# Optimization experiments

Hardware: AMD Instinct MI355X
Metric: run time of the kernel (lower is better)

## Reference

```python
import jax, jax.numpy as jnp
import numpy as np

D_MODEL = 1024
HEAD = 16


def setup_inputs() -> dict:
    key = jax.random.key(0)
    ks = jax.random.split(key, 11)
    B, S, D = 2, 2048, D_MODEL
    s = 1.0 / np.sqrt(D)
    return {
        "query": jax.random.normal(ks[0], (B, S, D), jnp.float32),
        "value": jax.random.normal(ks[1], (B, S, D), jnp.float32),
        "key": jax.random.normal(ks[2], (B, S, D), jnp.float32),
        "Wq_w": jax.random.normal(ks[3], (D, D), jnp.float32) * s,
        "Wq_b": jnp.zeros((D,), jnp.float32),
        "Wk_w": jax.random.normal(ks[4], (D, D), jnp.float32) * s,
        "Wk_b": jnp.zeros((D,), jnp.float32),
        "Wv_w": jax.random.normal(ks[5], (D, D), jnp.float32) * s,
        "Wv_b": jnp.zeros((D,), jnp.float32),
        "Wo_w": jax.random.normal(ks[6], (D, D), jnp.float32) * s,
        "Wo_b": jnp.zeros((D,), jnp.float32),
    }


def reference(query, value, key, Wq_w, Wq_b, Wk_w, Wk_b, Wv_w, Wv_b, Wo_w, Wo_b):
    B, S, D = query.shape
    H = HEAD
    kd = D // H
    # Linear projections (torch Linear: x @ W.T + b)
    Q = query @ Wq_w.T + Wq_b
    K = key @ Wk_w.T + Wk_b
    V = value @ Wv_w.T + Wv_b
    # [B, S, D] -> [B, H, S, kd]
    Q = Q.reshape(B, S, H, kd).transpose(0, 2, 1, 3)
    K = K.reshape(B, S, H, kd).transpose(0, 2, 1, 3)
    V = V.reshape(B, S, H, kd).transpose(0, 2, 1, 3)
    scale = 1.0 / jnp.sqrt(jnp.asarray(kd, query.dtype))
    score = jnp.einsum("bhqd,bhkd->bhqk", Q, K) * scale  # [B,H,S,S]
    attn = jax.nn.softmax(score, axis=-1)
    x = jnp.einsum("bhqk,bhkd->bhqd", attn, V)  # [B,H,S,kd]
    x = x.transpose(0, 2, 1, 3).reshape(B, S, D)
    return x @ Wo_w.T + Wo_b
```

## Files before the change

### kernel.cpp

```cpp
#include <hip/hip_runtime.h>
#include <stdint.h>
#include <stddef.h>


typedef __attribute__((ext_vector_type(8))) short short8;
typedef __attribute__((ext_vector_type(4))) float floatx4;
typedef __attribute__((ext_vector_type(16))) float f32x16;
typedef __attribute__((ext_vector_type(4))) unsigned short ushort4v;

#define MFMA16(a, b, c) __builtin_amdgcn_mfma_f32_16x16x32_bf16((a), (b), (c), 0, 0, 0)
#define MFMA32(a, b, c) __builtin_amdgcn_mfma_f32_32x32x16_bf16((a), (b), (c), 0, 0, 0)

#define CL2 0.18033688011112042f

__device__ __forceinline__ unsigned short f2bf(float f) {
  union { float f; unsigned u; } v; v.f = f;
  unsigned u = v.u;
  return (unsigned short)((u + 0x7fffu + ((u >> 16) & 1u)) >> 16);
}

__device__ __forceinline__ float fast_exp2(float x) {
  float r;
  asm("v_exp_f32 %0, %1" : "=v"(r) : "v"(x));
  return r;
}

__device__ __forceinline__ unsigned cvt_pk_bf16(float lo, float hi) {
  unsigned r;
  asm("v_cvt_pk_bf16_f32 %0, %1, %2" : "=v"(r) : "v"(lo), "v"(hi));
  return r;
}

#define PSWAP(a, b) asm("v_permlane32_swap_b32 %0, %1" : "+v"(a), "+v"(b))

#define WAITBAR(N) do { \
  asm volatile("s_waitcnt vmcnt(" #N ")" ::: "memory"); \
  __builtin_amdgcn_s_barrier(); \
  __builtin_amdgcn_sched_barrier(0); \
} while (0)

union B8 { unsigned short s[8]; short8 v; };
union U4 { unsigned w[4]; short8 v; };

__device__ __forceinline__ void gload_lds16(const unsigned short* g, unsigned short* l) {
  __builtin_amdgcn_global_load_lds(
      (__attribute__((address_space(1))) void*)(g),
      (__attribute__((address_space(3))) void*)(l), 16, 0, 0);
}

__global__ __launch_bounds__(256) void convert_all(
    const float* __restrict__ q, const float* __restrict__ k, const float* __restrict__ v,
    const float* __restrict__ wq, const float* __restrict__ wk,
    const float* __restrict__ wv, const float* __restrict__ wo,
    unsigned short* __restrict__ qb, unsigned short* __restrict__ kb,
    unsigned short* __restrict__ vb, unsigned short* __restrict__ w4)
{
  int b = blockIdx.x;
  const float* s; unsigned short* d;
  float sc = 1.0f;
  if (b < 2048)      { s = q;  d = qb; }
  else if (b < 4096) { s = k;  d = kb; b -= 2048; }
  else if (b < 6144) { s = v;  d = vb; b -= 4096; }
  else if (b < 6656) { s = wq; d = w4;            b -= 6144; sc = CL2; }
  else if (b < 7168) { s = wk; d = w4 + 1048576;  b -= 6656; }
  else if (b < 7680) { s = wv; d = w4 + 2097152;  b -= 7168; }
  else               { s = wo; d = w4 + 3145728;  b -= 7680; }
  const size_t i = ((size_t)b * 256 + threadIdx.x) * 8;
  float4 f0 = *(const float4*)(s + i);
  float4 f1 = *(const float4*)(s + i + 4);
  B8 u;
  u.s[0] = f2bf(f0.x * sc); u.s[1] = f2bf(f0.y * sc);
  u.s[2] = f2bf(f0.z * sc); u.s[3] = f2bf(f0.w * sc);
  u.s[4] = f2bf(f1.x * sc); u.s[5] = f2bf(f1.y * sc);
  u.s[6] = f2bf(f1.z * sc); u.s[7] = f2bf(f1.w * sc);
  *(short8*)(d + i) = u.v;
}

__global__ __launch_bounds__(256) void proj_gemm(
    const unsigned short* __restrict__ A0, const unsigned short* __restrict__ A1,
    const unsigned short* __restrict__ A2, const unsigned short* __restrict__ W4,
    const float* __restrict__ b0, const float* __restrict__ b1, const float* __restrict__ b2,
    unsigned short* __restrict__ Qp, unsigned short* __restrict__ Kp,
    unsigned short* __restrict__ Vt)
{
  const int z = blockIdx.z;
  const unsigned short* A = (z == 0) ? A0 : ((z == 1) ? A1 : A2);
  const unsigned short* W = W4 + (size_t)z * 1048576;
  const float* bias = (z == 0) ? b0 : ((z == 1) ? b1 : b2);
  const float esc = (z == 0) ? CL2 : 1.0f;

  const int m0 = blockIdx.y * 128;
  const int n0 = blockIdx.x * 128;
  const int tid = threadIdx.x;
  const int lane = tid & 63;
  const int wid = tid >> 6;
  const int wr = wid >> 1, wc = wid & 1;
  const int g = lane >> 4, l15 = lane & 15;

  __shared__ unsigned short As[3][128 * 32];
  __shared__ unsigned short Bs[3][128 * 32];

  const floatx4 vzero = {0.f, 0.f, 0.f, 0.f};
  floatx4 acc[4][4];
#pragma unroll
  for (int i = 0; i < 4; ++i)
#pragma unroll
    for (int j = 0; j < 4; ++j) acc[i][j] = vzero;

  const int lr = lane >> 2;
  const int lc = (lane & 3) * 8;
  const unsigned short* pa = &A[(size_t)(m0 + lr) * 1024 + lc];
  const unsigned short* pw = &W[(size_t)(n0 + lr) * 1024 + lc];
  const int rb0 = wid * 16, rb1 = (4 + wid) * 16;

#define PSTAGE(s_, b_) do { \
    gload_lds16(pa + (size_t)rb0 * 1024 + (s_) * 32, &As[b_][rb0 * 32]); \
    gload_lds16(pa + (size_t)rb1 * 1024 + (s_) * 32, &As[b_][rb1 * 32]); \
    gload_lds16(pw + (size_t)rb0 * 1024 + (s_) * 32, &Bs[b_][rb0 * 32]); \
    gload_lds16(pw + (size_t)rb1 * 1024 + (s_) * 32, &Bs[b_][rb1 * 32]); \
  } while (0)

  PSTAGE(0, 0);
  PSTAGE(1, 1);

  int cur = 0;
  for (int s = 0; s < 32; ++s) {
    if (s < 31) WAITBAR(4); else WAITBAR(0);
    if (s + 2 < 32) {
      int nb = cur + 2; if (nb >= 3) nb -= 3;
      PSTAGE(s + 2, nb);
    }

    short8 af[4], bfr[4];
#pragma unroll
    for (int mt = 0; mt < 4; ++mt)
      af[mt] = *(const short8*)&As[cur][(wr * 64 + mt * 16 + l15) * 32 + g * 8];
#pragma unroll
    for (int nt = 0; nt < 4; ++nt)
      bfr[nt] = *(const short8*)&Bs[cur][(wc * 64 + nt * 16 + l15) * 32 + g * 8];

    __builtin_amdgcn_s_setprio(1);
#pragma unroll
    for (int mt = 0; mt < 4; ++mt)
#pragma unroll
      for (int nt = 0; nt < 4; ++nt)
        acc[mt][nt] = MFMA16(af[mt], bfr[nt], acc[mt][nt]);
    __builtin_amdgcn_s_setprio(0);

    cur = (cur + 1 == 3) ? 0 : cur + 1;
  }
#undef PSTAGE

  float bvv[4];
#pragma unroll
  for (int nt = 0; nt < 4; ++nt) bvv[nt] = bias[n0 + wc * 64 + nt * 16 + l15] * esc;

  if (z < 2) {
    unsigned short* dst = (z == 0) ? Qp : Kp;
#pragma unroll
    for (int mt = 0; mt < 4; ++mt)
#pragma unroll
      for (int r = 0; r < 4; ++r) {
        const size_t row = (size_t)(m0 + wr * 64 + mt * 16 + g * 4 + r);
#pragma unroll
        for (int nt = 0; nt < 4; ++nt)
          dst[row * 1024 + n0 + wc * 64 + nt * 16 + l15] =
              f2bf(acc[mt][nt][r] + bvv[nt]);
      }
  } else {
#pragma unroll
    for (int mt = 0; mt < 4; ++mt) {
      const int sr = m0 + wr * 64 + mt * 16 + g * 4;
      const int bb = sr >> 11;
      const int ss = sr & 2047;
#pragma unroll
      for (int nt = 0; nt < 4; ++nt) {
        const int n = n0 + wc * 64 + nt * 16 + l15;
        const int hh = n >> 6, dd = n & 63;
        ushort4v o;
#pragma unroll
        for (int r = 0; r < 4; ++r) o[r] = f2bf(acc[mt][nt][r] + bvv[nt]);
        *(ushort4v*)&Vt[((size_t)(bb * 16 + hh) * 64 + dd) * 2048 + ss] = o;
      }
    }
  }
}

__global__ __launch_bounds__(256) void attn_kernel(
    const unsigned short* __restrict__ Qp, const unsigned short* __restrict__ Kp,
    const unsigned short* __restrict__ Vt, unsigned short* __restrict__ X)
{
  const int qb = blockIdx.x;
  const int bh = blockIdx.y;
  const int b = bh >> 4, h = bh & 15;
  const int tid = threadIdx.x, lane = tid & 63, w = tid >> 6;
  const int l31 = lane & 31, hi = lane >> 5;

  __shared__ unsigned short KV[3][2][4096];

  const int qrow = b * 2048 + qb * 128 + w * 32 + l31;
  short8 Qf[4];
#pragma unroll
  for (int ks = 0; ks < 4; ++ks)
    Qf[ks] = *(const short8*)&Qp[(size_t)qrow * 1024 + h * 64 + ks * 16 + hi * 8];

  const int s0 = tid, s1 = tid + 256;
  const int r0 = s0 >> 3, g0 = (s0 & 7) ^ (r0 & 7);
  const int r1 = s1 >> 3, g1 = (s1 & 7) ^ (r1 & 7);
  const unsigned short* kq0 = Kp + (size_t)(b * 2048 + r0) * 1024 + h * 64 + g0 * 8;
  const unsigned short* kq1 = Kp + (size_t)(b * 2048 + r1) * 1024 + h * 64 + g1 * 8;
  const unsigned short* vq0 = Vt + (size_t)(bh * 64 + r0) * 2048 + g0 * 8;
  const unsigned short* vq1 = Vt + (size_t)(bh * 64 + r1) * 2048 + g1 * 8;
  const int db0 = (w * 64) * 8;
  const int db1 = (256 + w * 64) * 8;

#define ASTAGE(t_, b_) do { \
    const size_t ko = (size_t)(t_) * 65536, vo = (size_t)(t_) * 64; \
    gload_lds16(kq0 + ko, &KV[b_][0][db0]); \
    gload_lds16(kq1 + ko, &KV[b_][0][db1]); \
    gload_lds16(vq0 + vo, &KV[b_][1][db0]); \
    gload_lds16(vq1 + vo, &KV[b_][1][db1]); \
  } while (0)

  f32x16 o0, o1;
#pragma unroll
  for (int i = 0; i < 16; ++i) { o0[i] = 0.f; o1[i] = 0.f; }
  float lp4[4] = {0.f, 0.f, 0.f, 0.f};

  ASTAGE(0, 0);
  ASTAGE(1, 1);

  int cur = 0;
  for (int t = 0; t < 32; ++t) {
    if (t < 31) WAITBAR(4); else WAITBAR(0);
    if (t + 2 < 32) {
      int nb = cur + 2; if (nb >= 3) nb -= 3;
      ASTAGE(t + 2, nb);
    }
    const unsigned short* Kb = &KV[cur][0][0];
    const unsigned short* Vb = &KV[cur][1][0];

    f32x16 c0, c1;
#pragma unroll
    for (int i = 0; i < 16; ++i) { c0[i] = 0.f; c1[i] = 0.f; }
    __builtin_amdgcn_s_setprio(1);
    {
      const int base = l31 * 64, kx = l31 & 7;
#pragma unroll
      for (int ks = 0; ks < 4; ++ks) {
        const short8 kf = *(const short8*)&Kb[base + (((ks * 2 + hi) ^ kx) << 3)];
        c0 = MFMA32(kf, Qf[ks], c0);
      }
    }
    {
      const int krow = 32 + l31;
      const int base = krow * 64, kx = krow & 7;
#pragma unroll
      for (int ks = 0; ks < 4; ++ks) {
        const short8 kf = *(const short8*)&Kb[base + (((ks * 2 + hi) ^ kx) << 3)];
        c1 = MFMA32(kf, Qf[ks], c1);
      }
    }
    __builtin_amdgcn_s_setprio(0);

    short8 vf0[4], vf1[4];
#pragma unroll
    for (int ks = 0; ks < 4; ++ks) {
      const int vx0 = l31 & 7;
      vf0[ks] = *(const short8*)&Vb[l31 * 64 + (((ks * 2 + hi) ^ vx0) << 3)];
      const int vrow = 32 + l31;
      vf1[ks] = *(const short8*)&Vb[vrow * 64 + (((ks * 2 + hi) ^ (vrow & 7)) << 3)];
    }

#pragma unroll
    for (int i = 0; i < 16; ++i) { c0[i] = fast_exp2(c0[i]); lp4[i & 3] += c0[i]; }
#pragma unroll
    for (int i = 0; i < 16; ++i) { c1[i] = fast_exp2(c1[i]); lp4[i & 3] += c1[i]; }

    short8 PA0, PA1, PA2, PA3;
    {
      unsigned p0 = cvt_pk_bf16(c0[0], c0[1]),   p1 = cvt_pk_bf16(c0[2], c0[3]);
      unsigned p2 = cvt_pk_bf16(c0[4], c0[5]),   p3 = cvt_pk_bf16(c0[6], c0[7]);
      unsigned p4 = cvt_pk_bf16(c0[8], c0[9]),   p5 = cvt_pk_bf16(c0[10], c0[11]);
      unsigned p6 = cvt_pk_bf16(c0[12], c0[13]), p7 = cvt_pk_bf16(c0[14], c0[15]);
      PSWAP(p0, p2); PSWAP(p1, p3); PSWAP(p4, p6); PSWAP(p5, p7);
      U4 a, bb_;
      a.w[0] = p0; a.w[1] = p1; a.w[2] = p2; a.w[3] = p3;          PA0 = a.v;
      bb_.w[0] = p4; bb_.w[1] = p5; bb_.w[2] = p6; bb_.w[3] = p7;  PA1 = bb_.v;
    }
    {
      unsigned p0 = cvt_pk_bf16(c1[0], c1[1]),   p1 = cvt_pk_bf16(c1[2], c1[3]);
      unsigned p2 = cvt_pk_bf16(c1[4], c1[5]),   p3 = cvt_pk_bf16(c1[6], c1[7]);
      unsigned p4 = cvt_pk_bf16(c1[8], c1[9]),   p5 = cvt_pk_bf16(c1[10], c1[11]);
      unsigned p6 = cvt_pk_bf16(c1[12], c1[13]), p7 = cvt_pk_bf16(c1[14], c1[15]);
      PSWAP(p0, p2); PSWAP(p1, p3); PSWAP(p4, p6); PSWAP(p5, p7);
      U4 a, bb_;
      a.w[0] = p0; a.w[1] = p1; a.w[2] = p2; a.w[3] = p3;          PA2 = a.v;
      bb_.w[0] = p4; bb_.w[1] = p5; bb_.w[2] = p6; bb_.w[3] = p7;  PA3 = bb_.v;
    }

    __builtin_amdgcn_s_setprio(1);
#pragma unroll
    for (int ks = 0; ks < 4; ++ks) {
      const short8 pa = (ks == 0) ? PA0 : (ks == 1) ? PA1 : (ks == 2) ? PA2 : PA3;
      o0 = MFMA32(vf0[ks], pa, o0);
      o1 = MFMA32(vf1[ks], pa, o1);
    }
    __builtin_amdgcn_s_setprio(0);

    cur = (cur + 1 == 3) ? 0 : cur + 1;
  }
#undef ASTAGE

  const float l_run = (lp4[0] + lp4[1]) + (lp4[2] + lp4[3]);
  const float l_tot = l_run + __shfl_xor(l_run, 32);
  const float linv = 1.f / l_tot;
#pragma unroll
  for (int a = 0; a < 4; ++a) {
    ushort4v v0, v1;
#pragma unroll
    for (int r = 0; r < 4; ++r) {
      v0[r] = f2bf(o0[a * 4 + r] * linv);
      v1[r] = f2bf(o1[a * 4 + r] * linv);
    }
    *(ushort4v*)&X[(size_t)qrow * 1024 + h * 64 + a * 8 + hi * 4] = v0;
    *(ushort4v*)&X[(size_t)qrow * 1024 + h * 64 + 32 + a * 8 + hi * 4] = v1;
  }
}

__global__ __launch_bounds__(256) void out_gemm(
    const unsigned short* __restrict__ A, const unsigned short* __restrict__ W,
    const float* __restrict__ bias, float* __restrict__ out)
{
  const int m0 = blockIdx.y * 64;
  const int n0 = blockIdx.x * 128;
  const int tid = threadIdx.x;
  const int lane = tid & 63;
  const int wid = tid >> 6;
  const int wr = wid >> 1, wc = wid & 1;
  const int g = lane >> 4, l15 = lane & 15;

  __shared__ unsigned short As[3][64 * 32];
  __shared__ unsigned short Bs[3][128 * 32];

  const floatx4 vzero = {0.f, 0.f, 0.f, 0.f};
  floatx4 acc[2][4];
#pragma unroll
  for (int i = 0; i < 2; ++i)
#pragma unroll
    for (int j = 0; j < 4; ++j) acc[i][j] = vzero;

  const int lr = lane >> 2;
  const int lc = (lane & 3) * 8;
  const unsigned short* pa = &A[(size_t)(m0 + lr) * 1024 + lc];
  const unsigned short* pw = &W[(size_t)(n0 + lr) * 1024 + lc];
  const int rb0 = wid * 16, rb1 = (4 + wid) * 16;

#define OSTAGE(s_, b_) do { \
    gload_lds16(pa + (size_t)rb0 * 1024 + (s_) * 32, &As[b_][rb0 * 32]); \
    gload_lds16(pw + (size_t)rb0 * 1024 + (s_) * 32, &Bs[b_][rb0 * 32]); \
    gload_lds16(pw + (size_t)rb1 * 1024 + (s_) * 32, &Bs[b_][rb1 * 32]); \
  } while (0)

  OSTAGE(0, 0);
  OSTAGE(1, 1);

  int cur = 0;
  for (int s = 0; s < 32; ++s) {
    if (s < 31) WAITBAR(3); else WAITBAR(0);
    if (s + 2 < 32) {
      int nb = cur + 2; if (nb >= 3) nb -= 3;
      OSTAGE(s + 2, nb);
    }

    short8 af[2], bfr[4];
#pragma unroll
    for (int mt = 0; mt < 2; ++mt)
      af[mt] = *(const short8*)&As[cur][(wr * 32 + mt * 16 + l15) * 32 + g * 8];
#pragma unroll
    for (int nt = 0; nt < 4; ++nt)
      bfr[nt] = *(const short8*)&Bs[cur][(wc * 64 + nt * 16 + l15) * 32 + g * 8];

    __builtin_amdgcn_s_setprio(1);
#pragma unroll
    for (int mt = 0; mt < 2; ++mt)
#pragma unroll
      for (int nt = 0; nt < 4; ++nt)
        acc[mt][nt] = MFMA16(af[mt], bfr[nt], acc[mt][nt]);
    __builtin_amdgcn_s_setprio(0);

    cur = (cur + 1 == 3) ? 0 : cur + 1;
  }
#undef OSTAGE

  float bvv[4];
#pragma unroll
  for (int nt = 0; nt < 4; ++nt) bvv[nt] = bias[n0 + wc * 64 + nt * 16 + l15];

#pragma unroll
  for (int mt = 0; mt < 2; ++mt)
#pragma unroll
    for (int r = 0; r < 4; ++r) {
      const size_t row = (size_t)(m0 + wr * 32 + mt * 16 + g * 4 + r);
#pragma unroll
      for (int nt = 0; nt < 4; ++nt)
        out[row * 1024 + n0 + wc * 64 + nt * 16 + l15] = acc[mt][nt][r] + bvv[nt];
    }
}

extern "C" void kernel_launch(void* const* d_in, const int* in_sizes, int n_in,
                              void* d_out, int out_size, void* d_ws, size_t ws_size,
                              hipStream_t stream)
{
  const float* query = (const float*)d_in[0];
  const float* value = (const float*)d_in[1];
  const float* key   = (const float*)d_in[2];
  const float* Wq = (const float*)d_in[3];
  const float* bq = (const float*)d_in[4];
  const float* Wk = (const float*)d_in[5];
  const float* bk = (const float*)d_in[6];
  const float* Wv = (const float*)d_in[7];
  const float* bv = (const float*)d_in[8];
  const float* Wo = (const float*)d_in[9];
  const float* bo = (const float*)d_in[10];
  float* out = (float*)d_out;

  const size_t M4 = (size_t)4096 * 1024;
  unsigned short* vb = (unsigned short*)d_ws;
  unsigned short* w4 = vb + M4;
  unsigned short* Qp = w4 + M4;
  unsigned short* Kp = Qp + M4;
  unsigned short* Vt = Kp + M4;
  unsigned short* X  = vb;
  unsigned short* qb = (unsigned short*)d_out;
  unsigned short* kb = qb + M4;

  dim3 blk(256);
  convert_all<<<8192, blk, 0, stream>>>(query, key, value, Wq, Wk, Wv, Wo,
                                        qb, kb, vb, w4);
  proj_gemm<<<dim3(8, 32, 3), blk, 0, stream>>>(qb, kb, vb, w4,
                                                bq, bk, bv, Qp, Kp, Vt);
  attn_kernel<<<dim3(16, 32), blk, 0, stream>>>(Qp, Kp, Vt, X);
  out_gemm<<<dim3(8, 64), blk, 0, stream>>>(X, w4 + 3 * 1048576, bo, out);
}
```

Measured before the change: 130.5 us.

## Swizzle GEMM LDS tiles, double-buffer attention with split accumulators and occupancy hint

The projection and output GEMMs now XOR-swizzle the 16-byte column groups, both in the global-to-LDS loads and in the fragment reads, to cut LDS bank conflicts. The attention kernel drops from a 3-stage to a 2-stage K/V LDS buffer synchronised with __syncthreads, and requests 2 blocks per CU via launch bounds. It also splits each MFMA accumulation chain into two independent accumulators that are summed before the exp and at the end, which shortens dependent MFMA chains. Shallower prefetch plus a full barrier each iteration may expose more load latency, and the register cap may cause spills.

```diff
diff --git a/kernel.cpp b/kernel.cpp
--- a/kernel.cpp
+++ b/kernel.cpp
@@ -108,16 +108,19 @@
     for (int j = 0; j < 4; ++j) acc[i][j] = vzero;
 
   const int lr = lane >> 2;
-  const int lc = (lane & 3) * 8;
-  const unsigned short* pa = &A[(size_t)(m0 + lr) * 1024 + lc];
-  const unsigned short* pw = &W[(size_t)(n0 + lr) * 1024 + lc];
   const int rb0 = wid * 16, rb1 = (4 + wid) * 16;
+  const int gsw0 = ((lane & 3) ^ (((rb0 + lr) >> 1) & 3)) * 8;
+  const int gsw1 = ((lane & 3) ^ (((rb1 + lr) >> 1) & 3)) * 8;
+  const unsigned short* pa0 = &A[(size_t)(m0 + rb0 + lr) * 1024 + gsw0];
+  const unsigned short* pa1 = &A[(size_t)(m0 + rb1 + lr) * 1024 + gsw1];
+  const unsigned short* pw0 = &W[(size_t)(n0 + rb0 + lr) * 1024 + gsw0];
+  const unsigned short* pw1 = &W[(size_t)(n0 + rb1 + lr) * 1024 + gsw1];
 
 #define PSTAGE(s_, b_) do { \
-    gload_lds16(pa + (size_t)rb0 * 1024 + (s_) * 32, &As[b_][rb0 * 32]); \
-    gload_lds16(pa + (size_t)rb1 * 1024 + (s_) * 32, &As[b_][rb1 * 32]); \
-    gload_lds16(pw + (size_t)rb0 * 1024 + (s_) * 32, &Bs[b_][rb0 * 32]); \
-    gload_lds16(pw + (size_t)rb1 * 1024 + (s_) * 32, &Bs[b_][rb1 * 32]); \
+    gload_lds16(pa0 + (s_) * 32, &As[b_][rb0 * 32]); \
+    gload_lds16(pa1 + (s_) * 32, &As[b_][rb1 * 32]); \
+    gload_lds16(pw0 + (s_) * 32, &Bs[b_][rb0 * 32]); \
+    gload_lds16(pw1 + (s_) * 32, &Bs[b_][rb1 * 32]); \
   } while (0)
 
   PSTAGE(0, 0);
@@ -133,11 +136,15 @@
 
     short8 af[4], bfr[4];
 #pragma unroll
-    for (int mt = 0; mt < 4; ++mt)
-      af[mt] = *(const short8*)&As[cur][(wr * 64 + mt * 16 + l15) * 32 + g * 8];
-#pragma unroll
-    for (int nt = 0; nt < 4; ++nt)
-      bfr[nt] = *(const short8*)&Bs[cur][(wc * 64 + nt * 16 + l15) * 32 + g * 8];
+    for (int mt = 0; mt < 4; ++mt) {
+      const int R = wr * 64 + mt * 16 + l15;
+      af[mt] = *(const short8*)&As[cur][R * 32 + ((g ^ ((R >> 1) & 3)) * 8)];
+    }
+#pragma unroll
+    for (int nt = 0; nt < 4; ++nt) {
+      const int R = wc * 64 + nt * 16 + l15;
+      bfr[nt] = *(const short8*)&Bs[cur][R * 32 + ((g ^ ((R >> 1) & 3)) * 8)];
+    }
 
     __builtin_amdgcn_s_setprio(1);
 #pragma unroll
@@ -186,7 +193,7 @@
   }
 }
 
-__global__ __launch_bounds__(256) void attn_kernel(
+__global__ __launch_bounds__(256, 2) void attn_kernel(
     const unsigned short* __restrict__ Qp, const unsigned short* __restrict__ Kp,
     const unsigned short* __restrict__ Vt, unsigned short* __restrict__ X)
 {
@@ -196,7 +203,7 @@
   const int tid = threadIdx.x, lane = tid & 63, w = tid >> 6;
   const int l31 = lane & 31, hi = lane >> 5;
 
-  __shared__ unsigned short KV[3][2][4096];
+  __shared__ unsigned short KV[2][2][4096];
 
   const int qrow = b * 2048 + qb * 128 + w * 32 + l31;
   short8 Qf[4];
@@ -214,103 +221,107 @@
   const int db0 = (w * 64) * 8;
   const int db1 = (256 + w * 64) * 8;
 
-#define ASTAGE(t_, b_) do { \
-    const size_t ko = (size_t)(t_) * 65536, vo = (size_t)(t_) * 64; \
-    gload_lds16(kq0 + ko, &KV[b_][0][db0]); \
-    gload_lds16(kq1 + ko, &KV[b_][0][db1]); \
-    gload_lds16(vq0 + vo, &KV[b_][1][db0]); \
-    gload_lds16(vq1 + vo, &KV[b_][1][db1]); \
-  } while (0)
-
-  f32x16 o0, o1;
-#pragma unroll
-  for (int i = 0; i < 16; ++i) { o0[i] = 0.f; o1[i] = 0.f; }
+  f32x16 o0a, o0b, o1a, o1b;
+#pragma unroll
+  for (int i = 0; i < 16; ++i) { o0a[i] = 0.f; o0b[i] = 0.f; o1a[i] = 0.f; o1b[i] = 0.f; }
   float lp4[4] = {0.f, 0.f, 0.f, 0.f};
 
-  ASTAGE(0, 0);
-  ASTAGE(1, 1);
+  gload_lds16(kq0, &KV[0][0][db0]);
+  gload_lds16(kq1, &KV[0][0][db1]);
+  gload_lds16(vq0, &KV[0][1][db0]);
+  gload_lds16(vq1, &KV[0][1][db1]);
+  __syncthreads();
 
   int cur = 0;
   for (int t = 0; t < 32; ++t) {
-    if (t < 31) WAITBAR(4); else WAITBAR(0);
-    if (t + 2 < 32) {
-      int nb = cur + 2; if (nb >= 3) nb -= 3;
-      ASTAGE(t + 2, nb);
+    if (t + 1 < 32) {
+      const size_t ko = (size_t)(t + 1) * 65536;
+      const size_t vo = (size_t)(t + 1) * 64;
+      gload_lds16(kq0 + ko, &KV[cur ^ 1][0][db0]);
+      gload_lds16(kq1 + ko, &KV[cur ^ 1][0][db1]);
+      gload_lds16(vq0 + vo, &KV[cur ^ 1][1][db0]);
+      gload_lds16(vq1 + vo, &KV[cur ^ 1][1][db1]);
     }
     const unsigned short* Kb = &KV[cur][0][0];
     const unsigned short* Vb = &KV[cur][1][0];
 
-    f32x16 c0, c1;
-#pragma unroll
-    for (int i = 0; i < 16; ++i) { c0[i] = 0.f; c1[i] = 0.f; }
-    __builtin_amdgcn_s_setprio(1);
+    f32x16 c0a, c0b, c1a, c1b;
+#pragma unroll
+    for (int i = 0; i < 16; ++i) { c0a[i] = 0.f; c0b[i] = 0.f; c1a[i] = 0.f; c1b[i] = 0.f; }
     {
-      const int base = l31 * 64, kx = l31 & 7;
+      const int kx = l31 & 7;
+      const int base0 = l31 * 64;
+      const int base1 = (32 + l31) * 64;
+      short8 kf00 = *(const short8*)&Kb[base0 + (((0 + hi) ^ kx) << 3)];
+      short8 kf01 = *(const short8*)&Kb[base0 + (((2 + hi) ^ kx) << 3)];
+      short8 kf02 = *(const short8*)&Kb[base0 + (((4 + hi) ^ kx) << 3)];
+      short8 kf03 = *(const short8*)&Kb[base0 + (((6 + hi) ^ kx) << 3)];
+      short8 kf10 = *(const short8*)&Kb[base1 + (((0 + hi) ^ kx) << 3)];
+      short8 kf11 = *(const short8*)&Kb[base1 + (((2 + hi) ^ kx) << 3)];
+      short8 kf12 = *(const short8*)&Kb[base1 + (((4 + hi) ^ kx) << 3)];
+      short8 kf13 = *(const short8*)&Kb[base1 + (((6 + hi) ^ kx) << 3)];
+      __builtin_amdgcn_s_setprio(1);
+      c0a = MFMA32(kf00, Qf[0], c0a); c0a = MFMA32(kf01, Qf[1], c0a);
+      c0b = MFMA32(kf02, Qf[2], c0b); c0b = MFMA32(kf03, Qf[3], c0b);
+      c1a = MFMA32(kf10, Qf[0], c1a); c1a = MFMA32(kf11, Qf[1], c1a);
+      c1b = MFMA32(kf12, Qf[2], c1b); c1b = MFMA32(kf13, Qf[3], c1b);
+      __builtin_amdgcn_s_setprio(0);
+    }
+
+    short8 vf0[4], vf1[4];
+    {
+      const int kx = l31 & 7;
+      const int vrow1 = 32 + l31;
 #pragma unroll
       for (int ks = 0; ks < 4; ++ks) {
-        const short8 kf = *(const short8*)&Kb[base + (((ks * 2 + hi) ^ kx) << 3)];
-        c0 = MFMA32(kf, Qf[ks], c0);
+        vf0[ks] = *(const short8*)&Vb[l31 * 64 + (((ks * 2 + hi) ^ kx) << 3)];
+        vf1[ks] = *(const short8*)&Vb[vrow1 * 64 + (((ks * 2 + hi) ^ (vrow1 & 7)) << 3)];
       }
     }
-    {
-      const int krow = 32 + l31;
-      const int base = krow * 64, kx = krow & 7;
-#pragma unroll
-      for (int ks = 0; ks < 4; ++ks) {
-        const short8 kf = *(const short8*)&Kb[base + (((ks * 2 + hi) ^ kx) << 3)];
-        c1 = MFMA32(kf, Qf[ks], c1);
-      }
-    }
-    __builtin_amdgcn_s_setprio(0);
-
-    short8 vf0[4], vf1[4];
-#pragma unroll
-    for (int ks = 0; ks < 4; ++ks) {
-      const int vx0 = l31 & 7;
-      vf0[ks] = *(const short8*)&Vb[l31 * 64 + (((ks * 2 + hi) ^ vx0) << 3)];
-      const int vrow = 32 + l31;
-      vf1[ks] = *(const short8*)&Vb[vrow * 64 + (((ks * 2 + hi) ^ (vrow & 7)) << 3)];
-    }
-
-#pragma unroll
-    for (int i = 0; i < 16; ++i) { c0[i] = fast_exp2(c0[i]); lp4[i & 3] += c0[i]; }
-#pragma unroll
-    for (int i = 0; i < 16; ++i) { c1[i] = fast_exp2(c1[i]); lp4[i & 3] += c1[i]; }
+
+#pragma unroll
+    for (int i = 0; i < 16; ++i) {
+      const float p = fast_exp2(c0a[i] + c0b[i]);
+      c0a[i] = p; lp4[i & 3] += p;
+    }
+#pragma unroll
+    for (int i = 0; i < 16; ++i) {
+      const float p = fast_exp2(c1a[i] + c1b[i]);
+      c1a[i] = p; lp4[i & 3] += p;
+    }
 
     short8 PA0, PA1, PA2, PA3;
     {
-      unsigned p0 = cvt_pk_bf16(c0[0], c0[1]),   p1 = cvt_pk_bf16(c0[2], c0[3]);
-      unsigned p2 = cvt_pk_bf16(c0[4], c0[5]),   p3 = cvt_pk_bf16(c0[6], c0[7]);
-      unsigned p4 = cvt_pk_bf16(c0[8], c0[9]),   p5 = cvt_pk_bf16(c0[10], c0[11]);
-      unsigned p6 = cvt_pk_bf16(c0[12], c0[13]), p7 = cvt_pk_bf16(c0[14], c0[15]);
+      unsigned p0 = cvt_pk_bf16(c0a[0], c0a[1]),   p1 = cvt_pk_bf16(c0a[2], c0a[3]);
+      unsigned p2 = cvt_pk_bf16(c0a[4], c0a[5]),   p3 = cvt_pk_bf16(c0a[6], c0a[7]);
+      unsigned p4 = cvt_pk_bf16(c0a[8], c0a[9]),   p5 = cvt_pk_bf16(c0a[10], c0a[11]);
+      unsigned p6 = cvt_pk_bf16(c0a[12], c0a[13]), p7 = cvt_pk_bf16(c0a[14], c0a[15]);
       PSWAP(p0, p2); PSWAP(p1, p3); PSWAP(p4, p6); PSWAP(p5, p7);
-      U4 a, bb_;
-      a.w[0] = p0; a.w[1] = p1; a.w[2] = p2; a.w[3] = p3;          PA0 = a.v;
-      bb_.w[0] = p4; bb_.w[1] = p5; bb_.w[2] = p6; bb_.w[3] = p7;  PA1 = bb_.v;
+      U4 a_, b_;
+      a_.w[0] = p0; a_.w[1] = p1; a_.w[2] = p2; a_.w[3] = p3;      PA0 = a_.v;
+      b_.w[0] = p4; b_.w[1] = p5; b_.w[2] = p6; b_.w[3] = p7;      PA1 = b_.v;
     }
     {
-      unsigned p0 = cvt_pk_bf16(c1[0], c1[1]),   p1 = cvt_pk_bf16(c1[2], c1[3]);
-      unsigned p2 = cvt_pk_bf16(c1[4], c1[5]),   p3 = cvt_pk_bf16(c1[6], c1[7]);
-      unsigned p4 = cvt_pk_bf16(c1[8], c1[9]),   p5 = cvt_pk_bf16(c1[10], c1[11]);
-      unsigned p6 = cvt_pk_bf16(c1[12], c1[13]), p7 = cvt_pk_bf16(c1[14], c1[15]);
+      unsigned p0 = cvt_pk_bf16(c1a[0], c1a[1]),   p1 = cvt_pk_bf16(c1a[2], c1a[3]);
+      unsigned p2 = cvt_pk_bf16(c1a[4], c1a[5]),   p3 = cvt_pk_bf16(c1a[6], c1a[7]);
+      unsigned p4 = cvt_pk_bf16(c1a[8], c1a[9]),   p5 = cvt_pk_bf16(c1a[10], c1a[11]);
+      unsigned p6 = cvt_pk_bf16(c1a[12], c1a[13]), p7 = cvt_pk_bf16(c1a[14], c1a[15]);
       PSWAP(p0, p2); PSWAP(p1, p3); PSWAP(p4, p6); PSWAP(p5, p7);
-      U4 a, bb_;
-      a.w[0] = p0; a.w[1] = p1; a.w[2] = p2; a.w[3] = p3;          PA2 = a.v;
-      bb_.w[0] = p4; bb_.w[1] = p5; bb_.w[2] = p6; bb_.w[3] = p7;  PA3 = bb_.v;
+      U4 a_, b_;
+      a_.w[0] = p0; a_.w[1] = p1; a_.w[2] = p2; a_.w[3] = p3;      PA2 = a_.v;
+      b_.w[0] = p4; b_.w[1] = p5; b_.w[2] = p6; b_.w[3] = p7;      PA3 = b_.v;
     }
 
     __builtin_amdgcn_s_setprio(1);
-#pragma unroll
-    for (int ks = 0; ks < 4; ++ks) {
-      const short8 pa = (ks == 0) ? PA0 : (ks == 1) ? PA1 : (ks == 2) ? PA2 : PA3;
-      o0 = MFMA32(vf0[ks], pa, o0);
-      o1 = MFMA32(vf1[ks], pa, o1);
-    }
+    o0a = MFMA32(vf0[0], PA0, o0a); o0a = MFMA32(vf0[1], PA1, o0a);
+    o0b = MFMA32(vf0[2], PA2, o0b); o0b = MFMA32(vf0[3], PA3, o0b);
+    o1a = MFMA32(vf1[0], PA0, o1a); o1a = MFMA32(vf1[1], PA1, o1a);
+    o1b = MFMA32(vf1[2], PA2, o1b); o1b = MFMA32(vf1[3], PA3, o1b);
     __builtin_amdgcn_s_setprio(0);
 
-    cur = (cur + 1 == 3) ? 0 : cur + 1;
+    __syncthreads();
+    cur ^= 1;
   }
-#undef ASTAGE
 
   const float l_run = (lp4[0] + lp4[1]) + (lp4[2] + lp4[3]);
   const float l_tot = l_run + __shfl_xor(l_run, 32);
@@ -320,8 +331,8 @@
     ushort4v v0, v1;
 #pragma unroll
     for (int r = 0; r < 4; ++r) {
-      v0[r] = f2bf(o0[a * 4 + r] * linv);
-      v1[r] = f2bf(o1[a * 4 + r] * linv);
+      v0[r] = f2bf((o0a[a * 4 + r] + o0b[a * 4 + r]) * linv);
+      v1[r] = f2bf((o1a[a * 4 + r] + o1b[a * 4 + r]) * linv);
     }
     *(ushort4v*)&X[(size_t)qrow * 1024 + h * 64 + a * 8 + hi * 4] = v0;
     *(ushort4v*)&X[(size_t)qrow * 1024 + h * 64 + 32 + a * 8 + hi * 4] = v1;
@@ -351,15 +362,17 @@
     for (int j = 0; j < 4; ++j) acc[i][j] = vzero;
 
   const int lr = lane >> 2;
-  const int lc = (lane & 3) * 8;
-  const unsigned short* pa = &A[(size_t)(m0 + lr) * 1024 + lc];
-  const unsigned short* pw = &W[(size_t)(n0 + lr) * 1024 + lc];
   const int rb0 = wid * 16, rb1 = (4 + wid) * 16;
+  const int gsw0 = ((lane & 3) ^ (((rb0 + lr) >> 1) & 3)) * 8;
+  const int gsw1 = ((lane & 3) ^ (((rb1 + lr) >> 1) & 3)) * 8;
+  const unsigned short* pa0 = &A[(size_t)(m0 + rb0 + lr) * 1024 + gsw0];
+  const unsigned short* pw0 = &W[(size_t)(n0 + rb0 + lr) * 1024 + gsw0];
+  const unsigned short* pw1 = &W[(size_t)(n0 + rb1 + lr) * 1024 + gsw1];
 
 #define OSTAGE(s_, b_) do { \
-    gload_lds16(pa + (size_t)rb0 * 1024 + (s_) * 32, &As[b_][rb0 * 32]); \
-    gload_lds16(pw + (size_t)rb0 * 1024 + (s_) * 32, &Bs[b_][rb0 * 32]); \
-    gload_lds16(pw + (size_t)rb1 * 1024 + (s_) * 32, &Bs[b_][rb1 * 32]); \
+    gload_lds16(pa0 + (s_) * 32, &As[b_][rb0 * 32]); \
+    gload_lds16(pw0 + (s_) * 32, &Bs[b_][rb0 * 32]); \
+    gload_lds16(pw1 + (s_) * 32, &Bs[b_][rb1 * 32]); \
   } while (0)
 
   OSTAGE(0, 0);
@@ -375,11 +388,15 @@
 
     short8 af[2], bfr[4];
 #pragma unroll
-    for (int mt = 0; mt < 2; ++mt)
-      af[mt] = *(const short8*)&As[cur][(wr * 32 + mt * 16 + l15) * 32 + g * 8];
-#pragma unroll
-    for (int nt = 0; nt < 4; ++nt)
-      bfr[nt] = *(const short8*)&Bs[cur][(wc * 64 + nt * 16 + l15) * 32 + g * 8];
+    for (int mt = 0; mt < 2; ++mt) {
+      const int R = wr * 32 + mt * 16 + l15;
+      af[mt] = *(const short8*)&As[cur][R * 32 + ((g ^ ((R >> 1) & 3)) * 8)];
+    }
+#pragma unroll
+    for (int nt = 0; nt < 4; ++nt) {
+      const int R = wc * 64 + nt * 16 + l15;
+      bfr[nt] = *(const short8*)&Bs[cur][R * 32 + ((g ^ ((R >> 1) & 3)) * 8)];
+    }
 
     __builtin_amdgcn_s_setprio(1);
 #pragma unroll
```

New measurement: 124.2 us. -4.8%, faster.
